# Performance work log

Hardware: AMD Instinct MI355X
Metric: run time of the kernel (lower is better)

The kernel has to match this reference:

```python
import jax, jax.numpy as jnp
import numpy as np

B, L, H, D = 64, 512, 512, 80  # batch, seq_len, hidden (size_list[3]), feature (size_list[0])


def setup_inputs() -> dict:
    key = jax.random.key(0)
    ks = jax.random.split(key, 12)
    s = 0.02
    return {
        "hid_r": jax.random.normal(ks[0], (B, L, H), jnp.float32),
        "in_mask": jnp.ones((B, L), jnp.bool_),
        "init_in": jnp.zeros((B, 1, D), jnp.float32),
        "h0": jnp.zeros((1, B, H), jnp.float32),
        "c0": jnp.zeros((1, B, H), jnp.float32),
        # lin_1: D -> H
        "W1": jax.random.normal(ks[1], (D, H), jnp.float32) * s,
        "b1": jnp.zeros((H,), jnp.float32),
        # LSTM cell (num_layers=1), PyTorch gate order i,f,g,o
        "W_ih": jax.random.normal(ks[2], (4 * H, H), jnp.float32) * s,
        "W_hh": jax.random.normal(ks[3], (4 * H, H), jnp.float32) * s,
        "b_ih": jnp.zeros((4 * H,), jnp.float32),
        "b_hh": jnp.zeros((4 * H,), jnp.float32),
        # ScaledDotProductAttention projections (q_in=kv_in=qk_out=v_out=H)
        "Wq": jax.random.normal(ks[4], (H, H), jnp.float32) * s,
        "bq": jnp.zeros((H,), jnp.float32),
        "Wk": jax.random.normal(ks[5], (H, H), jnp.float32) * s,
        "bk": jnp.zeros((H,), jnp.float32),
        "Wv": jax.random.normal(ks[6], (H, H), jnp.float32) * s,
        "bv": jnp.zeros((H,), jnp.float32),
        # lin_2: H -> D
        "W2": jax.random.normal(ks[7], (H, D), jnp.float32) * s,
        "b2": jnp.zeros((D,), jnp.float32),
    }


def _forward(hid_r, in_mask, init_in, h0, c0, W1, b1, W_ih, W_hh, b_ih, b_hh,
             Wq, bq, Wk, bk, Wv, bv, W2, b2):
    length = hid_r.shape[1]
    scale = 1.0 / jnp.sqrt(jnp.asarray(H, hid_r.dtype))
    # K/V projections don't depend on t; precompute (same math as per-step).
    K = jnp.einsum('blh,hk->blk', hid_r, Wk) + bk  # (B,L,H)
    V = jnp.einsum('blh,hk->blk', hid_r, Wv) + bv  # (B,L,H)
    neg = jnp.asarray(-1e9, hid_r.dtype)
    bias = b_ih + b_hh

    def step(carry, _):
        h, c, x_in = carry  # (B,H), (B,H), (B,D)
        x = jax.nn.relu(x_in @ W1 + b1)                       # lin_1 + ReLU
        gates = x @ W_ih.T + h @ W_hh.T + bias                # (B,4H)
        i, f, g, o = jnp.split(gates, 4, axis=-1)
        c = jax.nn.sigmoid(f) * c + jax.nn.sigmoid(i) * jnp.tanh(g)
        h = jax.nn.sigmoid(o) * jnp.tanh(c)
        q = h @ Wq + bq                                       # (B,H)
        scores = jnp.einsum('bh,blh->bl', q, K) * scale       # (B,L)
        scores = jnp.where(in_mask, scores, neg)
        attn = jax.nn.softmax(scores, axis=-1)                # (B,L)
        ctx = jnp.einsum('bl,blh->bh', attn, V)               # (B,H)
        out = ctx @ W2 + b2                                   # (B,D) -> next input
        return (h, c, out), (out, attn)

    init = (h0[0], c0[0], init_in[:, 0, :])
    _, (outs, attns) = jax.lax.scan(step, init, None, length=length)
    outputs = jnp.transpose(outs, (1, 0, 2))           # (B,L,D)
    attention_weights = jnp.transpose(attns, (1, 0, 2))  # (B,L,L)
    return outputs, attention_weights


def reference(hid_r, in_mask, init_in, h0, c0, W1, b1, W_ih, W_hh, b_ih, b_hh,
              Wq, bq, Wk, bk, Wv, bv, W2, b2):
    return _forward(hid_r, in_mask, init_in, h0, c0, W1, b1, W_ih, W_hh, b_ih, b_hh,
                    Wq, bq, Wk, bk, Wv, bv, W2, b2)
```

## Files before the change

kernel.cpp:

```cpp
#include <hip/hip_runtime.h>
#include <math.h>

#define B_ 64
#define L_ 512
#define H_ 512
#define D_ 80
#define NG 2048
#define SCALE 0.044194173824159216f

__device__ float g_K2[(size_t)B_ * L_ * H_];
__device__ float g_V2[(size_t)B_ * L_ * D_];
__device__ float g_sb[B_ * L_];
__device__ float g_WqT[H_ * H_];
__device__ float g_Wkq[H_ * H_];
__device__ float g_Wv2[H_ * D_];
__device__ float g_bkq[H_];
__device__ float g_bv2[D_];
__device__ float g_wkb[H_];
__device__ float g_bias[NG];
__device__ float g_c0s;
__device__ float g_xT[H_ * B_];
__device__ float g_hT[2][H_ * B_];
__device__ float g_hRM[B_ * H_];
__device__ float g_cT[H_ * B_];
__device__ float g_e[B_ * L_];
__device__ float g_psum[B_ * 8];

__global__ void k_prep_small(const float* __restrict__ Wq, const float* __restrict__ bk,
                             const float* __restrict__ bq, const float* __restrict__ Wk,
                             const float* __restrict__ bih, const float* __restrict__ bhh,
                             const float* __restrict__ bv, const float* __restrict__ W2) {
  __shared__ float red[256];
  int blk = blockIdx.x, tid = threadIdx.x;
  if (blk < 2) {
    int n = blk * 256 + tid;
    const float* wr = Wq + (size_t)n * H_;
    float s = 0.f;
    for (int j = 0; j < H_; ++j) s += bk[j] * wr[j];
    g_bkq[n] = s;
  } else if (blk < 4) {
    int m = (blk - 2) * 256 + tid;
    const float* wr = Wk + (size_t)m * H_;
    float s = 0.f;
    for (int k = 0; k < H_; ++k) s += wr[k] * bq[k];
    g_wkb[m] = s;
  } else if (blk < 12) {
    int j = (blk - 4) * 256 + tid;
    g_bias[j] = bih[j] + bhh[j];
  } else if (blk == 12) {
    if (tid < D_) {
      float s = 0.f;
      for (int k = 0; k < H_; ++k) s += bv[k] * W2[(size_t)k * D_ + tid];
      g_bv2[tid] = s;
    }
  } else {
    float s = 0.f;
    for (int k = tid; k < H_; k += 256) s += bk[k] * bq[k];
    red[tid] = s; __syncthreads();
    for (int o = 128; o > 0; o >>= 1) { if (tid < o) red[tid] += red[tid + o]; __syncthreads(); }
    if (tid == 0) g_c0s = red[0];
  }
}

__global__ void k_transpose_wq(const float* __restrict__ Wq) {
  int id = blockIdx.x * 256 + threadIdx.x;
  int j = id >> 9, n = id & (H_ - 1);
  g_WqT[(size_t)j * H_ + n] = Wq[(size_t)n * H_ + j];
}

__global__ void __launch_bounds__(256) k_gemm(const float* __restrict__ A,
                                              const float* __restrict__ Bext,
                                              int which, int M, int N, int K) {
  __shared__ __align__(16) float As[32][68];
  __shared__ __align__(16) float Bs[32][68];
  const float* Bm; const float* bias; float* C;
  switch (which) {
    case 0:  Bm = g_WqT; bias = nullptr; C = g_Wkq; break;
    case 1:  Bm = Bext;  bias = nullptr; C = g_Wv2; break;
    case 2:  Bm = g_Wkq; bias = g_bkq;   C = g_K2;  break;
    default: Bm = g_Wv2; bias = g_bv2;   C = g_V2;  break;
  }
  int bm = blockIdx.x, bn = blockIdx.y, tid = threadIdx.x;
  int tm = (tid & 15) << 2, tn = (tid >> 4) << 2;
  float acc[4][4] = {};
  for (int k0 = 0; k0 < K; k0 += 32) {
    for (int i = tid; i < 64 * 32; i += 256) {
      int m = i >> 5, kk = i & 31;
      As[kk][m] = A[(size_t)(bm * 64 + m) * K + k0 + kk];
    }
    for (int i = tid; i < 32 * 64; i += 256) {
      int kk = i >> 6, n = i & 63;
      int gn = bn * 64 + n;
      Bs[kk][n] = (gn < N) ? Bm[(size_t)(k0 + kk) * N + gn] : 0.f;
    }
    __syncthreads();
#pragma unroll 8
    for (int kk = 0; kk < 32; ++kk) {
      float4 av = *(const float4*)&As[kk][tm];
      float4 bv = *(const float4*)&Bs[kk][tn];
      float a[4] = {av.x, av.y, av.z, av.w};
      float bb[4] = {bv.x, bv.y, bv.z, bv.w};
#pragma unroll
      for (int i2 = 0; i2 < 4; ++i2)
#pragma unroll
        for (int j2 = 0; j2 < 4; ++j2) acc[i2][j2] += a[i2] * bb[j2];
    }
    __syncthreads();
  }
#pragma unroll
  for (int i2 = 0; i2 < 4; ++i2) {
    int gm = bm * 64 + tm + i2;
#pragma unroll
    for (int j2 = 0; j2 < 4; ++j2) {
      int gn = bn * 64 + tn + j2;
      if (gn < N) C[(size_t)gm * N + gn] = acc[i2][j2] + (bias ? bias[gn] : 0.f);
    }
  }
}

__global__ void k_sb(const float* __restrict__ hid) {
  __shared__ float wk[H_];
  int tid = threadIdx.x;
  for (int i = tid; i < H_; i += 256) wk[i] = g_wkb[i];
  __syncthreads();
  int wave = tid >> 6, lane = tid & 63;
  float c0s = g_c0s;
  int row0 = blockIdx.x * 32 + wave * 8;
  for (int r = 0; r < 8; ++r) {
    int row = row0 + r;
    const float* hr = hid + (size_t)row * H_;
    float s = 0.f;
#pragma unroll
    for (int j = 0; j < 8; ++j) { int k = lane + 64 * j; s += hr[k] * wk[k]; }
    for (int o = 32; o > 0; o >>= 1) s += __shfl_xor(s, o);
    if (lane == 0) g_sb[row] = s + c0s;
  }
}

__global__ void k_init(const float* __restrict__ h0, const float* __restrict__ c0,
                       const float* __restrict__ init_in, const float* __restrict__ W1,
                       const float* __restrict__ b1) {
  int blk = blockIdx.x, tid = threadIdx.x;
  if (blk < 128) {
    int id = blk * 256 + tid;
    int j = id >> 6, b = id & 63;
    g_hT[0][id] = h0[(size_t)b * H_ + j];
    g_cT[id]    = c0[(size_t)b * H_ + j];
  } else {
    int id = (blk - 128) * 256 + tid;
    int b = id >> 9, k = id & 511;
    const float* xi = init_in + (size_t)b * D_;
    float s = b1[k];
    for (int d = 0; d < D_; ++d) s += xi[d] * W1[(size_t)d * H_ + k];
    g_xT[(size_t)k * B_ + b] = fmaxf(s, 0.f);
  }
}

__global__ void __launch_bounds__(256) kA(const float* __restrict__ Wih,
                                          const float* __restrict__ Whh, int hp) {
  __shared__ float smg[4][B_];
  int blk = blockIdx.x, tid = threadIdx.x;
  int b = tid & 63, g = tid >> 6;
  const float* xT = g_xT;
  const float* hT = g_hT[hp];
  float* hTn = g_hT[hp ^ 1];
  for (int cc = 0; cc < 2; ++cc) {
    int col = blk * 2 + cc;
    int j = g * H_ + col;
    const float* wi = Wih + (size_t)j * H_;
    const float* wh = Whh + (size_t)j * H_;
    float ax0 = 0.f, ax1 = 0.f, ah0 = 0.f, ah1 = 0.f;
#pragma unroll 8
    for (int k = 0; k < H_; k += 2) {
      ax0 += xT[k * B_ + b] * wi[k];
      ah0 += hT[k * B_ + b] * wh[k];
      ax1 += xT[(k + 1) * B_ + b] * wi[k + 1];
      ah1 += hT[(k + 1) * B_ + b] * wh[k + 1];
    }
    smg[g][b] = g_bias[j] + ((ax0 + ax1) + (ah0 + ah1));
    __syncthreads();
    if (g == 0) {
      float iv = smg[0][b], fv = smg[1][b], gv = smg[2][b], ov = smg[3][b];
      float co = g_cT[col * B_ + b];
      float si = 1.f / (1.f + expf(-iv));
      float sf = 1.f / (1.f + expf(-fv));
      float so = 1.f / (1.f + expf(-ov));
      float cn = sf * co + si * tanhf(gv);
      float hn = so * tanhf(cn);
      g_cT[col * B_ + b] = cn;
      hTn[col * B_ + b]  = hn;
      g_hRM[(size_t)b * H_ + col] = hn;
    }
    __syncthreads();
  }
}

__global__ void __launch_bounds__(256) kC(const int* __restrict__ mask) {
  __shared__ __align__(16) float hs[H_];
  __shared__ float ps[4];
  int blk = blockIdx.x, tid = threadIdx.x;
  int b = blk >> 3, sub = blk & 7;
  for (int i = tid; i < H_; i += 256) hs[i] = g_hRM[(size_t)b * H_ + i];
  __syncthreads();
  int wave = tid >> 6, lane = tid & 63;
  const float* K2b = g_K2 + (size_t)b * L_ * H_;
  float4 h0 = *(const float4*)&hs[lane * 4];
  float4 h1 = *(const float4*)&hs[256 + lane * 4];
  float lsum = 0.f;
  int lbase = sub * 64 + wave * 16;
  for (int rg = 0; rg < 4; ++rg) {
    int l = lbase + rg * 4;
    float s[4];
#pragma unroll
    for (int r = 0; r < 4; ++r) {
      const float* rp = K2b + (size_t)(l + r) * H_ + lane * 4;
      float4 a0 = *(const float4*)rp;
      float4 a1 = *(const float4*)(rp + 256);
      s[r] = a0.x * h0.x + a0.y * h0.y + a0.z * h0.z + a0.w * h0.w
           + a1.x * h1.x + a1.y * h1.y + a1.z * h1.z + a1.w * h1.w;
    }
#pragma unroll
    for (int r = 0; r < 4; ++r) {
      float v = s[r];
      for (int o = 32; o > 0; o >>= 1) v += __shfl_xor(v, o);
      if (lane == 0) {
        int li = l + r;
        float sc = (v + g_sb[b * L_ + li]) * SCALE;
        float e = mask[b * L_ + li] ? expf(sc) : 0.f;
        g_e[b * L_ + li] = e;
        lsum += e;
      }
    }
  }
  if (lane == 0) ps[wave] = lsum;
  __syncthreads();
  if (tid == 0) g_psum[b * 8 + sub] = ps[0] + ps[1] + ps[2] + ps[3];
}

__global__ void __launch_bounds__(256) kDEF(int t, const float* __restrict__ W1,
                                            const float* __restrict__ b1,
                                            const float* __restrict__ b2,
                                            float* __restrict__ out) {
  __shared__ float at[L_];
  __shared__ float ot[D_];
  int b = blockIdx.x, tid = threadIdx.x;
  float S = 0.f;
#pragma unroll
  for (int i = 0; i < 8; ++i) S += g_psum[b * 8 + i];
  float inv = (S > 0.f) ? 1.f / S : 0.f;
  bool uni = !(S > 0.f);
  float* attn_out = out + (size_t)B_ * L_ * D_ + ((size_t)b * L_ + t) * L_;
  for (int l = tid; l < L_; l += 256) {
    float a = uni ? (1.f / L_) : g_e[b * L_ + l] * inv;
    at[l] = a;
    attn_out[l] = a;
  }
  __syncthreads();
  if (tid < D_) {
    const float* V2b = g_V2 + (size_t)b * L_ * D_ + tid;
    float a0 = 0.f, a1 = 0.f, a2 = 0.f, a3 = 0.f;
    for (int l = 0; l < L_; l += 4) {
      a0 += at[l]     * V2b[(size_t)l * D_];
      a1 += at[l + 1] * V2b[(size_t)(l + 1) * D_];
      a2 += at[l + 2] * V2b[(size_t)(l + 2) * D_];
      a3 += at[l + 3] * V2b[(size_t)(l + 3) * D_];
    }
    float acc = b2[tid] + ((a0 + a1) + (a2 + a3));
    ot[tid] = acc;
    out[((size_t)b * L_ + t) * D_ + tid] = acc;
  }
  __syncthreads();
  for (int k = tid; k < H_; k += 256) {
    float xv = b1[k];
#pragma unroll 8
    for (int d = 0; d < D_; ++d) xv += ot[d] * W1[(size_t)d * H_ + k];
    g_xT[(size_t)k * B_ + b] = fmaxf(xv, 0.f);
  }
}

extern "C" void kernel_launch(void* const* d_in, const int* in_sizes, int n_in,
                              void* d_out, int out_size, void* d_ws, size_t ws_size,
                              hipStream_t stream) {
  const float* hid  = (const float*)d_in[0];
  const int* mask = (const int*)d_in[1];
  const float* init_in = (const float*)d_in[2];
  const float* h0 = (const float*)d_in[3];
  const float* c0 = (const float*)d_in[4];
  const float* W1 = (const float*)d_in[5];
  const float* b1 = (const float*)d_in[6];
  const float* Wih = (const float*)d_in[7];
  const float* Whh = (const float*)d_in[8];
  const float* bih = (const float*)d_in[9];
  const float* bhh = (const float*)d_in[10];
  const float* Wq = (const float*)d_in[11];
  const float* bq = (const float*)d_in[12];
  const float* Wk = (const float*)d_in[13];
  const float* bk = (const float*)d_in[14];
  const float* Wv = (const float*)d_in[15];
  const float* bv = (const float*)d_in[16];
  const float* W2 = (const float*)d_in[17];
  const float* b2 = (const float*)d_in[18];
  float* out = (float*)d_out;

  k_prep_small<<<14, 256, 0, stream>>>(Wq, bk, bq, Wk, bih, bhh, bv, W2);
  k_transpose_wq<<<1024, 256, 0, stream>>>(Wq);
  k_gemm<<<dim3(8, 8), 256, 0, stream>>>(Wk, nullptr, 0, 512, 512, 512);
  k_gemm<<<dim3(8, 2), 256, 0, stream>>>(Wv, W2, 1, 512, 80, 512);
  k_gemm<<<dim3(512, 8), 256, 0, stream>>>(hid, nullptr, 2, 32768, 512, 512);
  k_gemm<<<dim3(512, 2), 256, 0, stream>>>(hid, nullptr, 3, 32768, 80, 512);
  k_sb<<<1024, 256, 0, stream>>>(hid);
  k_init<<<256, 256, 0, stream>>>(h0, c0, init_in, W1, b1);

  for (int t = 0; t < L_; ++t) {
    kA<<<256, 256, 0, stream>>>(Wih, Whh, t & 1);
    kC<<<512, 256, 0, stream>>>(mask);
    kDEF<<<64, 256, 0, stream>>>(t, W1, b1, b2, out);
  }
}
```

Baseline: 75.78 ms.

## Fuse per-step kernels into one persistent cooperative kernel with grid syncs

Replaces the 1536 per-timestep kernel launches with a single cooperative kernel of 256 blocks × 1024 threads that loops over time and separates phases with grid.sync(). It also transposes the projected V so the context reduction reads contiguously, and splits the gate work across 16 waves per block. Attention-weight writes move to separate blocks so they run alongside the context/lin_1 phase. The aim is to remove launch overhead and improve memory access. In exchange it adds three grid barriers per step and relies on the cooperative launch succeeding, falling back to the old kernels if it does not.

```diff
diff --git a/kernel.cpp b/kernel.cpp
--- a/kernel.cpp
+++ b/kernel.cpp
@@ -1,5 +1,8 @@
 #include <hip/hip_runtime.h>
+#include <hip/hip_cooperative_groups.h>
 #include <math.h>
+
+namespace cg = cooperative_groups;
 
 #define B_ 64
 #define L_ 512
@@ -9,7 +12,7 @@
 #define SCALE 0.044194173824159216f
 
 __device__ float g_K2[(size_t)B_ * L_ * H_];
-__device__ float g_V2[(size_t)B_ * L_ * D_];
+__device__ float g_V2T[(size_t)B_ * D_ * L_];
 __device__ float g_sb[B_ * L_];
 __device__ float g_WqT[H_ * H_];
 __device__ float g_Wkq[H_ * H_];
@@ -78,7 +81,7 @@
     case 0:  Bm = g_WqT; bias = nullptr; C = g_Wkq; break;
     case 1:  Bm = Bext;  bias = nullptr; C = g_Wv2; break;
     case 2:  Bm = g_Wkq; bias = g_bkq;   C = g_K2;  break;
-    default: Bm = g_Wv2; bias = g_bv2;   C = g_V2;  break;
+    default: Bm = g_Wv2; bias = g_bv2;   C = nullptr; break;
   }
   int bm = blockIdx.x, bn = blockIdx.y, tid = threadIdx.x;
   int tm = (tid & 15) << 2, tn = (tid >> 4) << 2;
@@ -113,7 +116,14 @@
 #pragma unroll
     for (int j2 = 0; j2 < 4; ++j2) {
       int gn = bn * 64 + tn + j2;
-      if (gn < N) C[(size_t)gm * N + gn] = acc[i2][j2] + (bias ? bias[gn] : 0.f);
+      if (gn >= N) continue;
+      float val = acc[i2][j2] + (bias ? bias[gn] : 0.f);
+      if (which == 3) {
+        int b = gm >> 9, l = gm & (L_ - 1);
+        g_V2T[((size_t)b * D_ + gn) * L_ + l] = val;
+      } else {
+        C[(size_t)gm * N + gn] = val;
+      }
     }
   }
 }
@@ -156,8 +166,159 @@
   }
 }
 
-__global__ void __launch_bounds__(256) kA(const float* __restrict__ Wih,
-                                          const float* __restrict__ Whh, int hp) {
+__global__ void __launch_bounds__(1024, 4) k_steps(
+    const float* __restrict__ Wih, const float* __restrict__ Whh,
+    const float* __restrict__ W1, const float* __restrict__ b1,
+    const float* __restrict__ b2, const int* __restrict__ mask,
+    float* __restrict__ out) {
+  cg::grid_group grid = cg::this_grid();
+  __shared__ float sm[16][B_];
+  __shared__ __align__(16) float hs[H_];
+  __shared__ float ps[16];
+  __shared__ float ot[D_];
+  __shared__ float Ssh[2];
+  const int blk = blockIdx.x, tid = threadIdx.x;
+  const int w = tid >> 6, lane = tid & 63;
+  int hp = 0;
+
+  for (int t = 0; t < L_; ++t) {
+    {
+      const int p = w & 1, g = (w >> 1) & 3, half = w >> 3;
+      const int c = blk * 2 + p;
+      const int j = g * H_ + c;
+      const float* Wrow = (half ? Whh : Wih) + (size_t)j * H_;
+      const float* src = half ? g_hT[hp] : g_xT;
+      const float4* W4 = (const float4*)Wrow;
+      float acc = 0.f;
+#pragma unroll 4
+      for (int k4 = 0; k4 < H_ / 4; ++k4) {
+        float4 wv = W4[k4];
+        int k = k4 * 4;
+        acc += wv.x * src[k * B_ + lane] + wv.y * src[(k + 1) * B_ + lane]
+             + wv.z * src[(k + 2) * B_ + lane] + wv.w * src[(k + 3) * B_ + lane];
+      }
+      sm[w][lane] = acc;
+      __syncthreads();
+      if (w < 2) {
+        const int c2 = blk * 2 + w;
+        float gv[4];
+#pragma unroll
+        for (int g2 = 0; g2 < 4; ++g2)
+          gv[g2] = sm[w | (g2 << 1)][lane] + sm[8 | w | (g2 << 1)][lane]
+                 + g_bias[g2 * H_ + c2];
+        float co = g_cT[c2 * B_ + lane];
+        float si = 1.f / (1.f + expf(-gv[0]));
+        float sf = 1.f / (1.f + expf(-gv[1]));
+        float so = 1.f / (1.f + expf(-gv[3]));
+        float cn = sf * co + si * tanhf(gv[2]);
+        float hn = so * tanhf(cn);
+        g_cT[c2 * B_ + lane] = cn;
+        g_hT[hp ^ 1][c2 * B_ + lane] = hn;
+        g_hRM[(size_t)lane * H_ + c2] = hn;
+      }
+    }
+    grid.sync();
+
+    {
+      const int b = blk >> 2, sub = blk & 3;
+      if (tid < H_) hs[tid] = g_hRM[(size_t)b * H_ + tid];
+      __syncthreads();
+      const float* K2b = g_K2 + (size_t)b * L_ * H_;
+      float4 h0 = *(const float4*)&hs[lane * 4];
+      float4 h1 = *(const float4*)&hs[256 + lane * 4];
+      float lsum = 0.f;
+      const int lbase = sub * 128 + w * 8;
+      for (int rg = 0; rg < 2; ++rg) {
+        int l0 = lbase + rg * 4;
+        float s[4];
+#pragma unroll
+        for (int r = 0; r < 4; ++r) {
+          const float* rp = K2b + (size_t)(l0 + r) * H_ + lane * 4;
+          float4 a0 = *(const float4*)rp;
+          float4 a1 = *(const float4*)(rp + 256);
+          s[r] = a0.x * h0.x + a0.y * h0.y + a0.z * h0.z + a0.w * h0.w
+               + a1.x * h1.x + a1.y * h1.y + a1.z * h1.z + a1.w * h1.w;
+        }
+#pragma unroll
+        for (int r = 0; r < 4; ++r) {
+          float v = s[r];
+          for (int o = 32; o > 0; o >>= 1) v += __shfl_xor(v, o);
+          if (lane == 0) {
+            int li = l0 + r;
+            float sc = (v + g_sb[b * L_ + li]) * SCALE;
+            float e = mask[b * L_ + li] ? expf(sc) : 0.f;
+            g_e[b * L_ + li] = e;
+            lsum += e;
+          }
+        }
+      }
+      if (lane == 0) ps[w] = lsum;
+      __syncthreads();
+      if (tid == 0) {
+        float S = 0.f;
+#pragma unroll
+        for (int i = 0; i < 16; ++i) S += ps[i];
+        g_psum[b * 4 + sub] = S;
+      }
+    }
+    grid.sync();
+
+    if (blk < B_) {
+      const int b = blk;
+      if (tid < L_) hs[tid] = g_e[b * L_ + tid];
+      if (tid == 0) {
+        float S = g_psum[b * 4] + g_psum[b * 4 + 1] + g_psum[b * 4 + 2] + g_psum[b * 4 + 3];
+        Ssh[0] = (S > 0.f) ? 1.f / S : 0.f;
+        Ssh[1] = (S > 0.f) ? 0.f : 1.f;
+      }
+      __syncthreads();
+      const float inv = Ssh[0];
+      const bool uni = Ssh[1] != 0.f;
+#pragma unroll
+      for (int i = 0; i < 5; ++i) {
+        const int d = w + 16 * i;
+        const float* vr = g_V2T + ((size_t)b * D_ + d) * L_;
+        float4 v0 = *(const float4*)&vr[lane * 8];
+        float4 v1 = *(const float4*)&vr[lane * 8 + 4];
+        float s;
+        if (uni) {
+          s = (v0.x + v0.y + v0.z + v0.w + v1.x + v1.y + v1.z + v1.w) * (1.f / L_);
+        } else {
+          float4 e0 = *(const float4*)&hs[lane * 8];
+          float4 e1 = *(const float4*)&hs[lane * 8 + 4];
+          s = e0.x * v0.x + e0.y * v0.y + e0.z * v0.z + e0.w * v0.w
+            + e1.x * v1.x + e1.y * v1.y + e1.z * v1.z + e1.w * v1.w;
+        }
+        for (int o = 32; o > 0; o >>= 1) s += __shfl_xor(s, o);
+        if (lane == 0) {
+          float val = (uni ? s : s * inv) + b2[d];
+          ot[d] = val;
+          out[((size_t)b * L_ + t) * D_ + d] = val;
+        }
+      }
+      __syncthreads();
+      if (tid < H_) {
+        float acc = b1[tid];
+        const float* w1c = W1 + tid;
+#pragma unroll 8
+        for (int d = 0; d < D_; ++d) acc += ot[d] * w1c[(size_t)d * H_];
+        g_xT[tid * B_ + b] = fmaxf(acc, 0.f);
+      }
+    } else if (blk < 2 * B_) {
+      const int b = blk - B_;
+      float S = g_psum[b * 4] + g_psum[b * 4 + 1] + g_psum[b * 4 + 2] + g_psum[b * 4 + 3];
+      float inv = (S > 0.f) ? 1.f / S : 0.f;
+      bool uni = !(S > 0.f);
+      float* ao = out + (size_t)B_ * L_ * D_ + ((size_t)b * L_ + t) * L_;
+      if (tid < L_) ao[tid] = uni ? (1.f / L_) : g_e[b * L_ + tid] * inv;
+    }
+    grid.sync();
+    hp ^= 1;
+  }
+}
+
+__global__ void __launch_bounds__(256) kA_fb(const float* __restrict__ Wih,
+                                             const float* __restrict__ Whh, int hp) {
   __shared__ float smg[4][B_];
   int blk = blockIdx.x, tid = threadIdx.x;
   int b = tid & 63, g = tid >> 6;
@@ -195,7 +356,7 @@
   }
 }
 
-__global__ void __launch_bounds__(256) kC(const int* __restrict__ mask) {
+__global__ void __launch_bounds__(256) kC_fb(const int* __restrict__ mask) {
   __shared__ __align__(16) float hs[H_];
   __shared__ float ps[4];
   int blk = blockIdx.x, tid = threadIdx.x;
@@ -237,10 +398,10 @@
   if (tid == 0) g_psum[b * 8 + sub] = ps[0] + ps[1] + ps[2] + ps[3];
 }
 
-__global__ void __launch_bounds__(256) kDEF(int t, const float* __restrict__ W1,
-                                            const float* __restrict__ b1,
-                                            const float* __restrict__ b2,
-                                            float* __restrict__ out) {
+__global__ void __launch_bounds__(256) kDEF_fb(int t, const float* __restrict__ W1,
+                                               const float* __restrict__ b1,
+                                               const float* __restrict__ b2,
+                                               float* __restrict__ out) {
   __shared__ float at[L_];
   __shared__ float ot[D_];
   int b = blockIdx.x, tid = threadIdx.x;
@@ -257,13 +418,13 @@
   }
   __syncthreads();
   if (tid < D_) {
-    const float* V2b = g_V2 + (size_t)b * L_ * D_ + tid;
+    const float* vr = g_V2T + ((size_t)b * D_ + tid) * L_;
     float a0 = 0.f, a1 = 0.f, a2 = 0.f, a3 = 0.f;
     for (int l = 0; l < L_; l += 4) {
-      a0 += at[l]     * V2b[(size_t)l * D_];
-      a1 += at[l + 1] * V2b[(size_t)(l + 1) * D_];
-      a2 += at[l + 2] * V2b[(size_t)(l + 2) * D_];
-      a3 += at[l + 3] * V2b[(size_t)(l + 3) * D_];
+      a0 += at[l] * vr[l];
+      a1 += at[l + 1] * vr[l + 1];
+      a2 += at[l + 2] * vr[l + 2];
+      a3 += at[l + 3] * vr[l + 3];
     }
     float acc = b2[tid] + ((a0 + a1) + (a2 + a3));
     ot[tid] = acc;
@@ -311,9 +472,15 @@
   k_sb<<<1024, 256, 0, stream>>>(hid);
   k_init<<<256, 256, 0, stream>>>(h0, c0, init_in, W1, b1);
 
-  for (int t = 0; t < L_; ++t) {
-    kA<<<256, 256, 0, stream>>>(Wih, Whh, t & 1);
-    kC<<<512, 256, 0, stream>>>(mask);
-    kDEF<<<64, 256, 0, stream>>>(t, W1, b1, b2, out);
-  }
-}
+  void* args[] = {(void*)&Wih, (void*)&Whh, (void*)&W1, (void*)&b1,
+                  (void*)&b2, (void*)&mask, (void*)&out};
+  hipError_t err = hipLaunchCooperativeKernel((const void*)k_steps, dim3(256),
+                                              dim3(1024), args, 0, stream);
+  if (err != hipSuccess) {
+    for (int t = 0; t < L_; ++t) {
+      kA_fb<<<256, 256, 0, stream>>>(Wih, Whh, t & 1);
+      kC_fb<<<512, 256, 0, stream>>>(mask);
+      kDEF_fb<<<64, 256, 0, stream>>>(t, W1, b1, b2, out);
+    }
+  }
+}
```

Measured after the change: 101.8 ms. 34.3% more time.
